# Kernel optimization log

Measured on AMD Instinct MI355X. Metric: run time of the kernel, lower is better.

## Reference

```python
import jax, jax.numpy as jnp
import numpy as np

# Config (matches AttentionConfig)
B, T, D = 2, 2048, 2048
H, KV, HD = 32, 8, 64          # n_heads, n_kv_heads, head_dim = d_model // n_heads
GROUPS = H // KV               # 4 query heads share each KV head
THETA = 10000.0
SCALE = 1.0 / np.sqrt(HD)
EPS = 1e-6


def setup_inputs() -> dict:
    key = jax.random.key(0)
    ks = jax.random.split(key, 6)
    def xavier(k, fan_in, fan_out):
        limit = np.sqrt(6.0 / (fan_in + fan_out))
        return jax.random.uniform(k, (fan_in, fan_out), jnp.float32, -limit, limit)
    return {
        "x": jax.random.normal(ks[0], (B, T, D), jnp.float32),
        "Wq": xavier(ks[1], D, H * HD),
        "Wk": xavier(ks[2], D, KV * HD),
        "Wv": xavier(ks[3], D, KV * HD),
        "Wo": xavier(ks[4], H * HD, D),
        "q_scale": jnp.ones((HD,), jnp.float32),
        "k_scale": jnp.ones((HD,), jnp.float32),
    }


def _rmsnorm(x, scale):
    # per-head RMSNorm over last dim (head_dim)
    rms = jnp.sqrt(jnp.mean(jnp.square(x), axis=-1, keepdims=True) + EPS)
    return (x / rms) * scale


def _rope(x):
    # x: (B, T, h, HD); rotate-half RoPE, offset=0
    pos = jnp.arange(x.shape[1], dtype=jnp.float32)
    inv_freq = 1.0 / (THETA ** (jnp.arange(0, HD, 2, dtype=jnp.float32) / HD))
    ang = pos[:, None] * inv_freq[None, :]          # (T, HD/2)
    cos = jnp.cos(ang)[None, :, None, :]
    sin = jnp.sin(ang)[None, :, None, :]
    x1, x2 = x[..., : HD // 2], x[..., HD // 2 :]
    return jnp.concatenate([x1 * cos - x2 * sin, x2 * cos + x1 * sin], axis=-1)


def reference(x, Wq, Wk, Wv, Wo, q_scale, k_scale):
    # projections -> (B, T, heads, HD)
    q = (x @ Wq).reshape(B, T, H, HD)
    k = (x @ Wk).reshape(B, T, KV, HD)
    v = (x @ Wv).reshape(B, T, KV, HD)
    # per-head QK RMSNorm (applied before RoPE, as in the module)
    q = _rmsnorm(q, q_scale)
    k = _rmsnorm(k, k_scale)
    # RoPE on q and k
    q = _rope(q)
    k = _rope(k)
    # repeat KV heads: head index = kv_head * GROUPS + g (matches _repeat_kv)
    k = jnp.repeat(k, GROUPS, axis=2)   # (B, T, H, HD)
    v = jnp.repeat(v, GROUPS, axis=2)
    # attention scores (B, H, T, T)
    logits = jnp.einsum("bqhd,bkhd->bhqk", q, k) * SCALE
    causal = jnp.triu(jnp.ones((T, T), bool), k=1)  # True = masked
    logits = jnp.where(causal[None, None], -jnp.inf, logits)
    w = jax.nn.softmax(logits, axis=-1)
    w = jnp.nan_to_num(w)
    out = jnp.einsum("bhqk,bkhd->bqhd", w, v).reshape(B, T, H * HD)
    return out @ Wo
```

## Files before the change

### kernel.cpp

```cpp
#include <hip/hip_runtime.h>
#include <hip/hip_bf16.h>

typedef __attribute__((ext_vector_type(4))) float f32x4;
typedef __attribute__((ext_vector_type(8))) short bf16x8;
typedef __attribute__((ext_vector_type(4))) short short4v;

#define DEVI __device__ __forceinline__

constexpr int Bc = 2, Tc = 2048, Dc = 2048, Hc = 32, KVc = 8, HDc = 64;
constexpr int GRP = Hc / KVc;
constexpr float EPSc = 1e-6f;
constexpr float QMULT = 0.125f * 1.4426950408889634f;
constexpr float INV2PI = 0.15915494309189535f;
constexpr float ROPE_C = 0.41524101186092029f;

DEVI short f2b(float f) {
    __hip_bfloat16 h = __float2bfloat16(f);
    short s;
    __builtin_memcpy(&s, &h, sizeof(short));
    return s;
}
DEVI float b2f(short s) {
    unsigned int u = ((unsigned int)(unsigned short)s) << 16;
    float f;
    __builtin_memcpy(&f, &u, sizeof(float));
    return f;
}

#define GLOAD16(g, l)                                                        \
    __builtin_amdgcn_global_load_lds(                                        \
        (const __attribute__((address_space(1))) void*)(g),                  \
        (__attribute__((address_space(3))) void*)(l), 16, 0, 0)

__global__ __launch_bounds__(256) void prep_all(const float* __restrict__ x,
                                                const float* __restrict__ Wq,
                                                const float* __restrict__ Wk,
                                                const float* __restrict__ Wv,
                                                const float* __restrict__ Wo,
                                                short* __restrict__ xb,
                                                short* __restrict__ WqkvT,
                                                short* __restrict__ WoT) {
    const int z = blockIdx.z;
    if (z == 4) {
        size_t base = ((size_t)(blockIdx.y * 32 + blockIdx.x) * 256 + threadIdx.x) * 8;
#pragma unroll
        for (int p = 0; p < 4; ++p) {
            size_t i = base + (size_t)p * 2097152;
            float4 a = *reinterpret_cast<const float4*>(x + i);
            float4 b = *reinterpret_cast<const float4*>(x + i + 4);
            bf16x8 o = {f2b(a.x), f2b(a.y), f2b(a.z), f2b(a.w),
                        f2b(b.x), f2b(b.y), f2b(b.z), f2b(b.w)};
            *reinterpret_cast<bf16x8*>(xb + i) = o;
        }
        return;
    }
    const float* src;
    short* dst;
    int C;
    if (z == 0)      { src = Wq; dst = WqkvT;                          C = 2048; }
    else if (z == 1) { src = Wk; dst = WqkvT + (size_t)2048 * 2048;    C = 512; }
    else if (z == 2) { src = Wv; dst = WqkvT + (size_t)2560 * 2048;    C = 512; }
    else             { src = Wo; dst = WoT;                            C = 2048; }
    const int n0 = blockIdx.x * 64, k0 = blockIdx.y * 64;
    if (n0 >= C) return;

    __shared__ __align__(16) short t[64][72];
    const int rl = threadIdx.x >> 2, q = threadIdx.x & 3;
#pragma unroll
    for (int jj = 0; jj < 4; ++jj) {
        float4 v = *reinterpret_cast<const float4*>(src + (size_t)(k0 + rl) * C + n0 + q * 16 + jj * 4);
        short4v s = {f2b(v.x), f2b(v.y), f2b(v.z), f2b(v.w)};
        *reinterpret_cast<short4v*>(&t[rl][q * 16 + jj * 4]) = s;
    }
    __syncthreads();
    alignas(16) short buf[16];
#pragma unroll
    for (int e = 0; e < 16; ++e) buf[e] = t[q * 16 + e][rl];
    short* d = dst + (size_t)(n0 + rl) * 2048 + k0 + q * 16;
    *reinterpret_cast<int4*>(d) = reinterpret_cast<int4*>(buf)[0];
    *reinterpret_cast<int4*>(d + 8) = reinterpret_cast<int4*>(buf)[1];
}

DEVI void xcd_swizzle(int nx, int& bx, int& by) {
    int nwg = nx * gridDim.y;
    int fb = by * nx + bx;
    int cpx = nwg >> 3;
    int swz = (fb & 7) * cpx + (fb >> 3);
    by = swz / nx;
    bx = swz - by * nx;
}

__global__ __launch_bounds__(256) void gemm_proj(const short* __restrict__ A,
                                                 const short* __restrict__ Bt,
                                                 const float* __restrict__ qs,
                                                 const float* __restrict__ ks,
                                                 short* __restrict__ qb,
                                                 short* __restrict__ kb,
                                                 short* __restrict__ vt) {
    constexpr int K = 2048;
    __shared__ __align__(16) short sA[2][128 * 64];
    __shared__ __align__(16) short sB[2][128 * 64];

    const int tid = threadIdx.x;
    const int wave = tid >> 6, lane = tid & 63;
    const int lhi = lane >> 4, llo = lane & 15;
    int bx = blockIdx.x, by = blockIdx.y;
    xcd_swizzle(24, bx, by);
    const int bm = by * 128, bn = bx * 128;
    const int wm = (wave >> 1) * 64, wn = (wave & 1) * 64;

    const short* apt[4];
    const short* bpt[4];
#pragma unroll
    for (int l = 0; l < 4; ++l) {
        int c = l * 256 + tid;
        int r = c >> 3, ck = (c & 7) ^ (r & 7);
        apt[l] = A + (size_t)(bm + r) * K + ck * 8;
        bpt[l] = Bt + (size_t)(bn + r) * K + ck * 8;
    }

    f32x4 acc[4][4] = {};

#pragma unroll
    for (int l = 0; l < 4; ++l) {
        GLOAD16(apt[l], &sA[0][(l * 256 + tid) * 8]);
        GLOAD16(bpt[l], &sB[0][(l * 256 + tid) * 8]);
    }
    int c = 0;
    const int co0 = ((lhi ^ (llo & 7)) << 3);
    const int co1 = (((4 + lhi) ^ (llo & 7)) << 3);

#pragma unroll 1
    for (int k0 = 0; k0 < K; k0 += 64) {
        if (k0 + 64 < K) {
            const int kn = k0 + 64;
#pragma unroll
            for (int l = 0; l < 4; ++l) {
                GLOAD16(apt[l] + kn, &sA[c ^ 1][(l * 256 + tid) * 8]);
                GLOAD16(bpt[l] + kn, &sB[c ^ 1][(l * 256 + tid) * 8]);
            }
            asm volatile("s_waitcnt vmcnt(8)" ::: "memory");
        } else {
            asm volatile("s_waitcnt vmcnt(0)" ::: "memory");
        }
        __builtin_amdgcn_s_barrier();
        asm volatile("" ::: "memory");

#pragma unroll
        for (int kk = 0; kk < 2; ++kk) {
            const int co = kk ? co1 : co0;
            bf16x8 af[4], bf[4];
#pragma unroll
            for (int i = 0; i < 4; ++i)
                af[i] = *reinterpret_cast<const bf16x8*>(&sA[c][(wm + i * 16 + llo) * 64 + co]);
#pragma unroll
            for (int j = 0; j < 4; ++j)
                bf[j] = *reinterpret_cast<const bf16x8*>(&sB[c][(wn + j * 16 + llo) * 64 + co]);
#pragma unroll
            for (int i = 0; i < 4; ++i)
#pragma unroll
                for (int j = 0; j < 4; ++j)
                    acc[i][j] = __builtin_amdgcn_mfma_f32_16x16x32_bf16(af[i], bf[j], acc[i][j], 0, 0, 0);
        }

        asm volatile("" ::: "memory");
        __builtin_amdgcn_s_barrier();
        c ^= 1;
    }

    const int rm = bm + wm;
    const int b = rm >> 11;
    const int tb = rm & 2047;
    const int col0 = bn + wn;

    if (col0 < 2560) {
        const bool isq = col0 < 2048;
        const float* scale = isq ? qs : ks;
        const float mult = isq ? QMULT : 1.0f;
        float scl[4];
#pragma unroll
        for (int j = 0; j < 4; ++j) scl[j] = scale[j * 16 + llo];
        short* outp;
        if (isq)
            outp = qb + (size_t)(b * Hc + (col0 >> 6)) * 2048 * 64;
        else
            outp = kb + (size_t)(b * KVc + ((col0 - 2048) >> 6)) * 2048 * 64;
        const float ir0 = INV2PI * exp2f(-ROPE_C * (float)llo);
        const float ir1 = INV2PI * exp2f(-ROPE_C * (float)(16 + llo));
#pragma unroll
        for (int i = 0; i < 4; ++i)
#pragma unroll
            for (int r = 0; r < 4; ++r) {
                float ss = 0.f;
#pragma unroll
                for (int j = 0; j < 4; ++j) ss += acc[i][j][r] * acc[i][j][r];
                ss += __shfl_xor(ss, 1);
                ss += __shfl_xor(ss, 2);
                ss += __shfl_xor(ss, 4);
                ss += __shfl_xor(ss, 8);
                float rinv = 1.0f / sqrtf(ss * (1.0f / 64.0f) + EPSc);
                float vn[4];
#pragma unroll
                for (int j = 0; j < 4; ++j) vn[j] = acc[i][j][r] * rinv * scl[j];
                const int t = tb + i * 16 + lhi * 4 + r;
                float f0 = (float)t * ir0;
                f0 -= floorf(f0);
                float f1 = (float)t * ir1;
                f1 -= floorf(f1);
                float sn0 = __builtin_amdgcn_sinf(f0), cs0 = __builtin_amdgcn_cosf(f0);
                float sn1 = __builtin_amdgcn_sinf(f1), cs1 = __builtin_amdgcn_cosf(f1);
                size_t base = (size_t)t * 64 + llo;
                outp[base]      = f2b((vn[0] * cs0 - vn[2] * sn0) * mult);
                outp[base + 16] = f2b((vn[1] * cs1 - vn[3] * sn1) * mult);
                outp[base + 32] = f2b((vn[2] * cs0 + vn[0] * sn0) * mult);
                outp[base + 48] = f2b((vn[3] * cs1 + vn[1] * sn1) * mult);
            }
    } else {
        const int kv = (col0 - 2560) >> 6;
        const int tile = tb >> 6;
        short* dst = vt + ((size_t)(b * 8 + kv) * 32 + tile) * 4096;
#pragma unroll
        for (int i = 0; i < 4; ++i)
#pragma unroll
            for (int j = 0; j < 4; ++j) {
                short4v p4 = {f2b(acc[i][j][0]), f2b(acc[i][j][1]),
                              f2b(acc[i][j][2]), f2b(acc[i][j][3])};
                *reinterpret_cast<short4v*>(
                    &dst[(j * 16 + llo) * 64 + i * 16 + lhi * 4]) = p4;
            }
    }
}

template <typename CT>
__global__ __launch_bounds__(256) void gemm_bt(const short* __restrict__ A,
                                               const short* __restrict__ Bt,
                                               CT* __restrict__ C, int M, int N, int K) {
    __shared__ __align__(16) short sA[2][128 * 64];
    __shared__ __align__(16) short sB[2][128 * 64];

    const int tid = threadIdx.x;
    const int wave = tid >> 6, lane = tid & 63;
    const int lhi = lane >> 4, llo = lane & 15;
    int bx = blockIdx.x, by = blockIdx.y;
    xcd_swizzle(gridDim.x, bx, by);
    const int bm = by * 128, bn = bx * 128;
    const int wm = (wave >> 1) * 64, wn = (wave & 1) * 64;

    const short* apt[4];
    const short* bpt[4];
#pragma unroll
    for (int l = 0; l < 4; ++l) {
        int c = l * 256 + tid;
        int r = c >> 3, ck = (c & 7) ^ (r & 7);
        apt[l] = A + (size_t)(bm + r) * K + ck * 8;
        bpt[l] = Bt + (size_t)(bn + r) * K + ck * 8;
    }

    f32x4 acc[4][4] = {};

#pragma unroll
    for (int l = 0; l < 4; ++l) {
        GLOAD16(apt[l], &sA[0][(l * 256 + tid) * 8]);
        GLOAD16(bpt[l], &sB[0][(l * 256 + tid) * 8]);
    }
    int c = 0;
    const int co0 = ((lhi ^ (llo & 7)) << 3);
    const int co1 = (((4 + lhi) ^ (llo & 7)) << 3);

#pragma unroll 1
    for (int k0 = 0; k0 < K; k0 += 64) {
        if (k0 + 64 < K) {
            const int kn = k0 + 64;
#pragma unroll
            for (int l = 0; l < 4; ++l) {
                GLOAD16(apt[l] + kn, &sA[c ^ 1][(l * 256 + tid) * 8]);
                GLOAD16(bpt[l] + kn, &sB[c ^ 1][(l * 256 + tid) * 8]);
            }
            asm volatile("s_waitcnt vmcnt(8)" ::: "memory");
        } else {
            asm volatile("s_waitcnt vmcnt(0)" ::: "memory");
        }
        __builtin_amdgcn_s_barrier();
        asm volatile("" ::: "memory");

#pragma unroll
        for (int kk = 0; kk < 2; ++kk) {
            const int co = kk ? co1 : co0;
            bf16x8 af[4], bf[4];
#pragma unroll
            for (int i = 0; i < 4; ++i)
                af[i] = *reinterpret_cast<const bf16x8*>(&sA[c][(wm + i * 16 + llo) * 64 + co]);
#pragma unroll
            for (int j = 0; j < 4; ++j)
                bf[j] = *reinterpret_cast<const bf16x8*>(&sB[c][(wn + j * 16 + llo) * 64 + co]);
#pragma unroll
            for (int i = 0; i < 4; ++i)
#pragma unroll
                for (int j = 0; j < 4; ++j)
                    acc[i][j] = __builtin_amdgcn_mfma_f32_16x16x32_bf16(af[i], bf[j], acc[i][j], 0, 0, 0);
        }

        asm volatile("" ::: "memory");
        __builtin_amdgcn_s_barrier();
        c ^= 1;
    }

#pragma unroll
    for (int i = 0; i < 4; ++i)
#pragma unroll
        for (int j = 0; j < 4; ++j)
#pragma unroll
            for (int r = 0; r < 4; ++r) {
                size_t idx = (size_t)(bm + wm + i * 16 + lhi * 4 + r) * N + bn + wn + j * 16 + llo;
                if constexpr (sizeof(CT) == 2)
                    C[idx] = f2b(acc[i][j][r]);
                else
                    C[idx] = acc[i][j][r];
            }
}

__global__ __launch_bounds__(256) void attn_fwd(const short* __restrict__ Qb,
                                                const short* __restrict__ Kb,
                                                const short* __restrict__ Vt,
                                                short* __restrict__ Ob) {
    __shared__ __align__(16) short sK[2][64 * 64];
    __shared__ __align__(16) short sV[2][64 * 64];
    __shared__ __align__(16) short sP[4][32 * 72];

    const int hb = blockIdx.x;
    const int qt = 15 - (int)blockIdx.y;
    const int h = hb & 31, b = hb >> 5;
    const int kvh = h >> 2;
    const int tid = threadIdx.x, wave = tid >> 6, lane = tid & 63;
    const int lhi = lane >> 4, llo = lane & 15;

    const short* Qp = Qb + (size_t)(b * Hc + h) * Tc * 64;
    const short* Kp = Kb + (size_t)(b * KVc + kvh) * Tc * 64;
    const short* Vp = Vt + (size_t)(b * KVc + kvh) * 32 * 4096;

    const int srow0 = tid >> 3, sslot0 = tid & 7;
    const int srow1 = (256 + tid) >> 3, sslot1 = tid & 7;
    const int soff0 = (sslot0 ^ (srow0 & 7)) * 8;
    const int soff1 = (sslot1 ^ (srow1 & 7)) * 8;

    const int Q0 = qt * 128 + wave * 32;
    const int ktmax_w = (Q0 + 31) >> 6;
    const int nkt = 2 * qt + 2;

    bf16x8 qf[2][2];
#pragma unroll
    for (int q16 = 0; q16 < 2; ++q16)
#pragma unroll
        for (int kk = 0; kk < 2; ++kk)
            qf[q16][kk] = *reinterpret_cast<const bf16x8*>(
                Qp + (size_t)(Q0 + q16 * 16 + llo) * 64 + kk * 32 + lhi * 8);

    f32x4 o[2][4] = {};
    float mreg[2] = {-1e30f, -1e30f};
    float lreg[2] = {0.f, 0.f};

    {
        GLOAD16(Kp + (size_t)srow0 * 64 + soff0, &sK[0][tid * 8]);
        GLOAD16(Vp + (size_t)srow0 * 64 + soff0, &sV[0][tid * 8]);
        GLOAD16(Kp + (size_t)srow1 * 64 + soff1, &sK[0][(256 + tid) * 8]);
        GLOAD16(Vp + (size_t)srow1 * 64 + soff1, &sV[0][(256 + tid) * 8]);
    }
    int c = 0;

#pragma unroll 1
    for (int kt = 0; kt < nkt; ++kt) {
        const bool has_next = (kt + 1) < nkt;
        if (has_next) {
            const size_t kbase = (size_t)(kt + 1) * 4096;
            GLOAD16(Kp + kbase + srow0 * 64 + soff0, &sK[c ^ 1][tid * 8]);
            GLOAD16(Vp + kbase + srow0 * 64 + soff0, &sV[c ^ 1][tid * 8]);
            GLOAD16(Kp + kbase + srow1 * 64 + soff1, &sK[c ^ 1][(256 + tid) * 8]);
            GLOAD16(Vp + kbase + srow1 * 64 + soff1, &sV[c ^ 1][(256 + tid) * 8]);
            asm volatile("s_waitcnt vmcnt(4)" ::: "memory");
        } else {
            asm volatile("s_waitcnt vmcnt(0)" ::: "memory");
        }
        __builtin_amdgcn_s_barrier();
        asm volatile("" ::: "memory");

        if (kt <= ktmax_w) {
            const short* sKc = sK[c];
            const short* sVc = sV[c];
            f32x4 st[2][4];
            __builtin_amdgcn_s_setprio(1);
#pragma unroll
            for (int n = 0; n < 4; ++n) {
                int krow = n * 16 + llo;
                bf16x8 ka0 = *reinterpret_cast<const bf16x8*>(
                    &sKc[krow * 64 + ((lhi ^ (krow & 7)) << 3)]);
                bf16x8 ka1 = *reinterpret_cast<const bf16x8*>(
                    &sKc[krow * 64 + (((4 + lhi) ^ (krow & 7)) << 3)]);
                f32x4 z = {0.f, 0.f, 0.f, 0.f};
                st[0][n] = __builtin_amdgcn_mfma_f32_16x16x32_bf16(ka0, qf[0][0], z, 0, 0, 0);
                st[0][n] = __builtin_amdgcn_mfma_f32_16x16x32_bf16(ka1, qf[0][1], st[0][n], 0, 0, 0);
                st[1][n] = __builtin_amdgcn_mfma_f32_16x16x32_bf16(ka0, qf[1][0], z, 0, 0, 0);
                st[1][n] = __builtin_amdgcn_mfma_f32_16x16x32_bf16(ka1, qf[1][1], st[1][n], 0, 0, 0);
            }
            __builtin_amdgcn_s_setprio(0);
            if (kt == ktmax_w) {
#pragma unroll
                for (int q16 = 0; q16 < 2; ++q16) {
                    int qg = Q0 + q16 * 16 + llo;
#pragma unroll
                    for (int n = 0; n < 4; ++n)
#pragma unroll
                        for (int r = 0; r < 4; ++r) {
                            int kvg = kt * 64 + n * 16 + lhi * 4 + r;
                            if (kvg > qg) st[q16][n][r] = -1e30f;
                        }
                }
            }
            float pm[2];
#pragma unroll
            for (int q16 = 0; q16 < 2; ++q16) {
                float r0 = fmaxf(fmaxf(st[q16][0][0], st[q16][0][1]),
                                 fmaxf(st[q16][0][2], st[q16][0][3]));
                float r1 = fmaxf(fmaxf(st[q16][1][0], st[q16][1][1]),
                                 fmaxf(st[q16][1][2], st[q16][1][3]));
                float r2 = fmaxf(fmaxf(st[q16][2][0], st[q16][2][1]),
                                 fmaxf(st[q16][2][2], st[q16][2][3]));
                float r3 = fmaxf(fmaxf(st[q16][3][0], st[q16][3][1]),
                                 fmaxf(st[q16][3][2], st[q16][3][3]));
                float p = fmaxf(fmaxf(r0, r1), fmaxf(r2, r3));
                p = fmaxf(p, __shfl_xor(p, 16));
                p = fmaxf(p, __shfl_xor(p, 32));
                pm[q16] = p;
            }
            bool defer = __all((pm[0] - mreg[0] <= 8.f) && (pm[1] - mreg[1] <= 8.f));
            if (!defer) {
                float alpha[2];
#pragma unroll
                for (int q16 = 0; q16 < 2; ++q16) {
                    float mn = fmaxf(mreg[q16], pm[q16]);
                    alpha[q16] = __builtin_amdgcn_exp2f(mreg[q16] - mn);
                    mreg[q16] = mn;
                    lreg[q16] *= alpha[q16];
                }
#pragma unroll
                for (int q16 = 0; q16 < 2; ++q16)
#pragma unroll
                    for (int r = 0; r < 4; ++r) {
                        float ar = __shfl(alpha[q16], lhi * 4 + r);
#pragma unroll
                        for (int j = 0; j < 4; ++j) o[q16][j][r] *= ar;
                    }
            }
#pragma unroll
            for (int q16 = 0; q16 < 2; ++q16) {
                float ps = 0.f;
#pragma unroll
                for (int n = 0; n < 4; ++n)
#pragma unroll
                    for (int r = 0; r < 4; ++r) {
                        float p = __builtin_amdgcn_exp2f(st[q16][n][r] - mreg[q16]);
                        st[q16][n][r] = p;
                        ps += p;
                    }
                ps += __shfl_xor(ps, 16);
                ps += __shfl_xor(ps, 32);
                lreg[q16] += ps;
            }
#pragma unroll
            for (int q16 = 0; q16 < 2; ++q16)
#pragma unroll
                for (int n = 0; n < 4; ++n) {
                    short4v p4 = {f2b(st[q16][n][0]), f2b(st[q16][n][1]),
                                  f2b(st[q16][n][2]), f2b(st[q16][n][3])};
                    *reinterpret_cast<short4v*>(
                        &sP[wave][(q16 * 16 + llo) * 72 + n * 16 + lhi * 4]) = p4;
                }
            __builtin_amdgcn_s_setprio(1);
#pragma unroll
            for (int kk = 0; kk < 2; ++kk) {
                bf16x8 pa0 = *reinterpret_cast<const bf16x8*>(
                    &sP[wave][(0 * 16 + llo) * 72 + kk * 32 + lhi * 8]);
                bf16x8 pa1 = *reinterpret_cast<const bf16x8*>(
                    &sP[wave][(1 * 16 + llo) * 72 + kk * 32 + lhi * 8]);
#pragma unroll
                for (int j = 0; j < 4; ++j) {
                    int vrow = j * 16 + llo;
                    bf16x8 vf = *reinterpret_cast<const bf16x8*>(
                        &sVc[vrow * 64 + ((((kk * 4) + lhi) ^ (vrow & 7)) << 3)]);
                    o[0][j] = __builtin_amdgcn_mfma_f32_16x16x32_bf16(pa0, vf, o[0][j], 0, 0, 0);
                    o[1][j] = __builtin_amdgcn_mfma_f32_16x16x32_bf16(pa1, vf, o[1][j], 0, 0, 0);
                }
            }
            __builtin_amdgcn_s_setprio(0);
        }
        asm volatile("" ::: "memory");
        __builtin_amdgcn_s_barrier();
        c ^= 1;
    }

#pragma unroll
    for (int q16 = 0; q16 < 2; ++q16) {
        float inv = 1.0f / lreg[q16];
#pragma unroll
        for (int r = 0; r < 4; ++r) {
            float ivr = __shfl(inv, lhi * 4 + r);
            int qrow = Q0 + q16 * 16 + lhi * 4 + r;
#pragma unroll
            for (int j = 0; j < 4; ++j)
                Ob[((size_t)(b * Tc + qrow)) * 2048 + h * 64 + j * 16 + llo] =
                    f2b(o[q16][j][r] * ivr);
        }
    }
}

extern "C" void kernel_launch(void* const* d_in, const int* in_sizes, int n_in,
                              void* d_out, int out_size, void* d_ws, size_t ws_size,
                              hipStream_t stream) {
    const float* x  = (const float*)d_in[0];
    const float* Wq = (const float*)d_in[1];
    const float* Wk = (const float*)d_in[2];
    const float* Wv = (const float*)d_in[3];
    const float* Wo = (const float*)d_in[4];
    const float* qs = (const float*)d_in[5];
    const float* ks = (const float*)d_in[6];
    float* out = (float*)d_out;

    char* w = (char*)d_ws;
    short* xb    = (short*)(w);
    short* WqkvT = (short*)(w + 16777216);
    short* WoT   = (short*)(w + 29360128);
    short* vt    = (short*)(w + 37748736);
    short* qb    = (short*)(w + 62914560);
    short* kb    = (short*)(w + 79691776);
    short* ob    = xb;

    dim3 blk(256);
    prep_all<<<dim3(32, 32, 5), blk, 0, stream>>>(x, Wq, Wk, Wv, Wo, xb, WqkvT, WoT);
    gemm_proj<<<dim3(24, 32), blk, 0, stream>>>(xb, WqkvT, qs, ks, qb, kb, vt);
    attn_fwd<<<dim3(64, 16), blk, 0, stream>>>(qb, kb, vt, ob);
    gemm_bt<float><<<dim3(16, 32), blk, 0, stream>>>(ob, WoT, out, 4096, 2048, 2048);
}
```

Measured before the change: 218.5 us.

## Transpose attention probabilities via cross-lane shuffles instead of LDS staging

Replaces the per-wave shared-memory round trip for the softmax probability tile (write as C layout, read back as A-operand layout) with in-register bf16 packing and __shfl-based lane permutation. It also drops the sP LDS buffer and adds a min-blocks-per-CU hint of 4 to launch bounds. The aim is to cut LDS traffic and the store-load latency on the inner loop and free LDS for occupancy. The cost is more shuffle instructions (each a ds_bpermute) plus selects, and possible register pressure from the occupancy hint.

```diff
diff --git a/kernel.cpp b/kernel.cpp
--- a/kernel.cpp
+++ b/kernel.cpp
@@ -319,13 +319,12 @@
             }
 }
 
-__global__ __launch_bounds__(256) void attn_fwd(const short* __restrict__ Qb,
-                                                const short* __restrict__ Kb,
-                                                const short* __restrict__ Vt,
-                                                short* __restrict__ Ob) {
+__global__ __launch_bounds__(256, 4) void attn_fwd(const short* __restrict__ Qb,
+                                                   const short* __restrict__ Kb,
+                                                   const short* __restrict__ Vt,
+                                                   short* __restrict__ Ob) {
     __shared__ __align__(16) short sK[2][64 * 64];
     __shared__ __align__(16) short sV[2][64 * 64];
-    __shared__ __align__(16) short sP[4][32 * 72];
 
     const int hb = blockIdx.x;
     const int qt = 15 - (int)blockIdx.y;
@@ -346,6 +345,10 @@
     const int Q0 = qt * 128 + wave * 32;
     const int ktmax_w = (Q0 + 31) >> 6;
     const int nkt = 2 * qt + 2;
+
+    const int src0 = llo + ((lhi & 1) << 5);
+    const int src1 = src0 + 16;
+    const bool nsel = (lhi & 2) != 0;
 
     bf16x8 qf[2][2];
 #pragma unroll
@@ -465,22 +468,34 @@
                 ps += __shfl_xor(ps, 32);
                 lreg[q16] += ps;
             }
-#pragma unroll
-            for (int q16 = 0; q16 < 2; ++q16)
-#pragma unroll
-                for (int n = 0; n < 4; ++n) {
-                    short4v p4 = {f2b(st[q16][n][0]), f2b(st[q16][n][1]),
-                                  f2b(st[q16][n][2]), f2b(st[q16][n][3])};
-                    *reinterpret_cast<short4v*>(
-                        &sP[wave][(q16 * 16 + llo) * 72 + n * 16 + lhi * 4]) = p4;
-                }
+            unsigned w0[2][4], w1[2][4];
+#pragma unroll
+            for (int q16 = 0; q16 < 2; ++q16) {
+                unsigned pk[4][2];
+#pragma unroll
+                for (int n = 0; n < 4; ++n)
+#pragma unroll
+                    for (int p = 0; p < 2; ++p)
+                        pk[n][p] = (unsigned)(unsigned short)f2b(st[q16][n][2 * p]) |
+                                   ((unsigned)(unsigned short)f2b(st[q16][n][2 * p + 1]) << 16);
+#pragma unroll
+                for (int kk = 0; kk < 2; ++kk)
+#pragma unroll
+                    for (int e2 = 0; e2 < 4; ++e2) {
+                        int src = (e2 < 2) ? src0 : src1;
+                        unsigned lo = __shfl((int)pk[2 * kk + 0][e2 & 1], src);
+                        unsigned hi = __shfl((int)pk[2 * kk + 1][e2 & 1], src);
+                        unsigned v = nsel ? hi : lo;
+                        if (q16 == 0) w0[kk][e2] = v;
+                        else          w1[kk][e2] = v;
+                    }
+            }
             __builtin_amdgcn_s_setprio(1);
 #pragma unroll
             for (int kk = 0; kk < 2; ++kk) {
-                bf16x8 pa0 = *reinterpret_cast<const bf16x8*>(
-                    &sP[wave][(0 * 16 + llo) * 72 + kk * 32 + lhi * 8]);
-                bf16x8 pa1 = *reinterpret_cast<const bf16x8*>(
-                    &sP[wave][(1 * 16 + llo) * 72 + kk * 32 + lhi * 8]);
+                bf16x8 pa0, pa1;
+                __builtin_memcpy(&pa0, w0[kk], 16);
+                __builtin_memcpy(&pa1, w1[kk], 16);
 #pragma unroll
                 for (int j = 0; j < 4; ++j) {
                     int vrow = j * 16 + llo;
```

After: 246.5 us. +12.8%, slower.

## Split attention work across eight waves of sixteen query rows each

Applied to the files above, without the earlier changes.

The attention kernel moves from 256 threads with 4 waves, each handling 32 query rows, to 512 threads with 8 waves, each handling 16 rows. Each thread now issues one K and one V tile load per stage, and the per-wave softmax state and accumulators shrink. The goal is more wave-level parallelism and lower register pressure for better latency hiding. In exchange, each wave reads the K/V fragments from LDS for only 16 rows instead of 32, which raises LDS traffic per unit of MFMA work, and blocks become larger.

```diff
diff --git a/kernel.cpp b/kernel.cpp
--- a/kernel.cpp
+++ b/kernel.cpp
@@ -319,13 +319,13 @@
             }
 }
 
-__global__ __launch_bounds__(256) void attn_fwd(const short* __restrict__ Qb,
+__global__ __launch_bounds__(512) void attn_fwd(const short* __restrict__ Qb,
                                                 const short* __restrict__ Kb,
                                                 const short* __restrict__ Vt,
                                                 short* __restrict__ Ob) {
     __shared__ __align__(16) short sK[2][64 * 64];
     __shared__ __align__(16) short sV[2][64 * 64];
-    __shared__ __align__(16) short sP[4][32 * 72];
+    __shared__ __align__(16) short sP[8][16 * 72];
 
     const int hb = blockIdx.x;
     const int qt = 15 - (int)blockIdx.y;
@@ -338,32 +338,26 @@
     const short* Kp = Kb + (size_t)(b * KVc + kvh) * Tc * 64;
     const short* Vp = Vt + (size_t)(b * KVc + kvh) * 32 * 4096;
 
-    const int srow0 = tid >> 3, sslot0 = tid & 7;
-    const int srow1 = (256 + tid) >> 3, sslot1 = tid & 7;
-    const int soff0 = (sslot0 ^ (srow0 & 7)) * 8;
-    const int soff1 = (sslot1 ^ (srow1 & 7)) * 8;
-
-    const int Q0 = qt * 128 + wave * 32;
-    const int ktmax_w = (Q0 + 31) >> 6;
+    const int srow = tid >> 3, sslot = tid & 7;
+    const int soff = (sslot ^ (srow & 7)) * 8;
+
+    const int Q0 = qt * 128 + wave * 16;
+    const int ktmax_w = (Q0 + 15) >> 6;
     const int nkt = 2 * qt + 2;
 
-    bf16x8 qf[2][2];
-#pragma unroll
-    for (int q16 = 0; q16 < 2; ++q16)
-#pragma unroll
-        for (int kk = 0; kk < 2; ++kk)
-            qf[q16][kk] = *reinterpret_cast<const bf16x8*>(
-                Qp + (size_t)(Q0 + q16 * 16 + llo) * 64 + kk * 32 + lhi * 8);
-
-    f32x4 o[2][4] = {};
-    float mreg[2] = {-1e30f, -1e30f};
-    float lreg[2] = {0.f, 0.f};
+    bf16x8 qf[2];
+#pragma unroll
+    for (int kk = 0; kk < 2; ++kk)
+        qf[kk] = *reinterpret_cast<const bf16x8*>(
+            Qp + (size_t)(Q0 + llo) * 64 + kk * 32 + lhi * 8);
+
+    f32x4 o[4] = {};
+    float mreg = -1e30f;
+    float lreg = 0.f;
 
     {
-        GLOAD16(Kp + (size_t)srow0 * 64 + soff0, &sK[0][tid * 8]);
-        GLOAD16(Vp + (size_t)srow0 * 64 + soff0, &sV[0][tid * 8]);
-        GLOAD16(Kp + (size_t)srow1 * 64 + soff1, &sK[0][(256 + tid) * 8]);
-        GLOAD16(Vp + (size_t)srow1 * 64 + soff1, &sV[0][(256 + tid) * 8]);
+        GLOAD16(Kp + (size_t)srow * 64 + soff, &sK[0][tid * 8]);
+        GLOAD16(Vp + (size_t)srow * 64 + soff, &sV[0][tid * 8]);
     }
     int c = 0;
 
@@ -372,11 +366,9 @@
         const bool has_next = (kt + 1) < nkt;
         if (has_next) {
             const size_t kbase = (size_t)(kt + 1) * 4096;
-            GLOAD16(Kp + kbase + srow0 * 64 + soff0, &sK[c ^ 1][tid * 8]);
-            GLOAD16(Vp + kbase + srow0 * 64 + soff0, &sV[c ^ 1][tid * 8]);
-            GLOAD16(Kp + kbase + srow1 * 64 + soff1, &sK[c ^ 1][(256 + tid) * 8]);
-            GLOAD16(Vp + kbase + srow1 * 64 + soff1, &sV[c ^ 1][(256 + tid) * 8]);
-            asm volatile("s_waitcnt vmcnt(4)" ::: "memory");
+            GLOAD16(Kp + kbase + srow * 64 + soff, &sK[c ^ 1][tid * 8]);
+            GLOAD16(Vp + kbase + srow * 64 + soff, &sV[c ^ 1][tid * 8]);
+            asm volatile("s_waitcnt vmcnt(2)" ::: "memory");
         } else {
             asm volatile("s_waitcnt vmcnt(0)" ::: "memory");
         }
@@ -386,7 +378,7 @@
         if (kt <= ktmax_w) {
             const short* sKc = sK[c];
             const short* sVc = sV[c];
-            f32x4 st[2][4];
+            f32x4 st[4];
             __builtin_amdgcn_s_setprio(1);
 #pragma unroll
             for (int n = 0; n < 4; ++n) {
@@ -396,98 +388,68 @@
                 bf16x8 ka1 = *reinterpret_cast<const bf16x8*>(
                     &sKc[krow * 64 + (((4 + lhi) ^ (krow & 7)) << 3)]);
                 f32x4 z = {0.f, 0.f, 0.f, 0.f};
-                st[0][n] = __builtin_amdgcn_mfma_f32_16x16x32_bf16(ka0, qf[0][0], z, 0, 0, 0);
-                st[0][n] = __builtin_amdgcn_mfma_f32_16x16x32_bf16(ka1, qf[0][1], st[0][n], 0, 0, 0);
-                st[1][n] = __builtin_amdgcn_mfma_f32_16x16x32_bf16(ka0, qf[1][0], z, 0, 0, 0);
-                st[1][n] = __builtin_amdgcn_mfma_f32_16x16x32_bf16(ka1, qf[1][1], st[1][n], 0, 0, 0);
+                st[n] = __builtin_amdgcn_mfma_f32_16x16x32_bf16(ka0, qf[0], z, 0, 0, 0);
+                st[n] = __builtin_amdgcn_mfma_f32_16x16x32_bf16(ka1, qf[1], st[n], 0, 0, 0);
             }
             __builtin_amdgcn_s_setprio(0);
             if (kt == ktmax_w) {
-#pragma unroll
-                for (int q16 = 0; q16 < 2; ++q16) {
-                    int qg = Q0 + q16 * 16 + llo;
-#pragma unroll
-                    for (int n = 0; n < 4; ++n)
-#pragma unroll
-                        for (int r = 0; r < 4; ++r) {
-                            int kvg = kt * 64 + n * 16 + lhi * 4 + r;
-                            if (kvg > qg) st[q16][n][r] = -1e30f;
-                        }
+                int qg = Q0 + llo;
+#pragma unroll
+                for (int n = 0; n < 4; ++n)
+#pragma unroll
+                    for (int r = 0; r < 4; ++r) {
+                        int kvg = kt * 64 + n * 16 + lhi * 4 + r;
+                        if (kvg > qg) st[n][r] = -1e30f;
+                    }
+            }
+            float r0 = fmaxf(fmaxf(st[0][0], st[0][1]), fmaxf(st[0][2], st[0][3]));
+            float r1 = fmaxf(fmaxf(st[1][0], st[1][1]), fmaxf(st[1][2], st[1][3]));
+            float r2 = fmaxf(fmaxf(st[2][0], st[2][1]), fmaxf(st[2][2], st[2][3]));
+            float r3 = fmaxf(fmaxf(st[3][0], st[3][1]), fmaxf(st[3][2], st[3][3]));
+            float pm = fmaxf(fmaxf(r0, r1), fmaxf(r2, r3));
+            pm = fmaxf(pm, __shfl_xor(pm, 16));
+            pm = fmaxf(pm, __shfl_xor(pm, 32));
+            bool defer = __all(pm - mreg <= 8.f);
+            if (!defer) {
+                float mn = fmaxf(mreg, pm);
+                float alpha = __builtin_amdgcn_exp2f(mreg - mn);
+                mreg = mn;
+                lreg *= alpha;
+#pragma unroll
+                for (int r = 0; r < 4; ++r) {
+                    float ar = __shfl(alpha, lhi * 4 + r);
+#pragma unroll
+                    for (int j = 0; j < 4; ++j) o[j][r] *= ar;
                 }
             }
-            float pm[2];
-#pragma unroll
-            for (int q16 = 0; q16 < 2; ++q16) {
-                float r0 = fmaxf(fmaxf(st[q16][0][0], st[q16][0][1]),
-                                 fmaxf(st[q16][0][2], st[q16][0][3]));
-                float r1 = fmaxf(fmaxf(st[q16][1][0], st[q16][1][1]),
-                                 fmaxf(st[q16][1][2], st[q16][1][3]));
-                float r2 = fmaxf(fmaxf(st[q16][2][0], st[q16][2][1]),
-                                 fmaxf(st[q16][2][2], st[q16][2][3]));
-                float r3 = fmaxf(fmaxf(st[q16][3][0], st[q16][3][1]),
-                                 fmaxf(st[q16][3][2], st[q16][3][3]));
-                float p = fmaxf(fmaxf(r0, r1), fmaxf(r2, r3));
-                p = fmaxf(p, __shfl_xor(p, 16));
-                p = fmaxf(p, __shfl_xor(p, 32));
-                pm[q16] = p;
-            }
-            bool defer = __all((pm[0] - mreg[0] <= 8.f) && (pm[1] - mreg[1] <= 8.f));
-            if (!defer) {
-                float alpha[2];
-#pragma unroll
-                for (int q16 = 0; q16 < 2; ++q16) {
-                    float mn = fmaxf(mreg[q16], pm[q16]);
-                    alpha[q16] = __builtin_amdgcn_exp2f(mreg[q16] - mn);
-                    mreg[q16] = mn;
-                    lreg[q16] *= alpha[q16];
+            float ps = 0.f;
+#pragma unroll
+            for (int n = 0; n < 4; ++n)
+#pragma unroll
+                for (int r = 0; r < 4; ++r) {
+                    float p = __builtin_amdgcn_exp2f(st[n][r] - mreg);
+                    st[n][r] = p;
+                    ps += p;
                 }
-#pragma unroll
-                for (int q16 = 0; q16 < 2; ++q16)
-#pragma unroll
-                    for (int r = 0; r < 4; ++r) {
-                        float ar = __shfl(alpha[q16], lhi * 4 + r);
-#pragma unroll
-                        for (int j = 0; j < 4; ++j) o[q16][j][r] *= ar;
-                    }
-            }
-#pragma unroll
-            for (int q16 = 0; q16 < 2; ++q16) {
-                float ps = 0.f;
-#pragma unroll
-                for (int n = 0; n < 4; ++n)
-#pragma unroll
-                    for (int r = 0; r < 4; ++r) {
-                        float p = __builtin_amdgcn_exp2f(st[q16][n][r] - mreg[q16]);
-                        st[q16][n][r] = p;
-                        ps += p;
-                    }
-                ps += __shfl_xor(ps, 16);
-                ps += __shfl_xor(ps, 32);
-                lreg[q16] += ps;
-            }
-#pragma unroll
-            for (int q16 = 0; q16 < 2; ++q16)
-#pragma unroll
-                for (int n = 0; n < 4; ++n) {
-                    short4v p4 = {f2b(st[q16][n][0]), f2b(st[q16][n][1]),
-                                  f2b(st[q16][n][2]), f2b(st[q16][n][3])};
-                    *reinterpret_cast<short4v*>(
-                        &sP[wave][(q16 * 16 + llo) * 72 + n * 16 + lhi * 4]) = p4;
-                }
+            ps += __shfl_xor(ps, 16);
+            ps += __shfl_xor(ps, 32);
+            lreg += ps;
+#pragma unroll
+            for (int n = 0; n < 4; ++n) {
+                short4v p4 = {f2b(st[n][0]), f2b(st[n][1]), f2b(st[n][2]), f2b(st[n][3])};
+                *reinterpret_cast<short4v*>(&sP[wave][llo * 72 + n * 16 + lhi * 4]) = p4;
+            }
             __builtin_amdgcn_s_setprio(1);
 #pragma unroll
             for (int kk = 0; kk < 2; ++kk) {
-                bf16x8 pa0 = *reinterpret_cast<const bf16x8*>(
-                    &sP[wave][(0 * 16 + llo) * 72 + kk * 32 + lhi * 8]);
-                bf16x8 pa1 = *reinterpret_cast<const bf16x8*>(
-                    &sP[wave][(1 * 16 + llo) * 72 + kk * 32 + lhi * 8]);
+                bf16x8 pa = *reinterpret_cast<const bf16x8*>(
+                    &sP[wave][llo * 72 + kk * 32 + lhi * 8]);
 #pragma unroll
                 for (int j = 0; j < 4; ++j) {
                     int vrow = j * 16 + llo;
                     bf16x8 vf = *reinterpret_cast<const bf16x8*>(
                         &sVc[vrow * 64 + ((((kk * 4) + lhi) ^ (vrow & 7)) << 3)]);
-                    o[0][j] = __builtin_amdgcn_mfma_f32_16x16x32_bf16(pa0, vf, o[0][j], 0, 0, 0);
-                    o[1][j] = __builtin_amdgcn_mfma_f32_16x16x32_bf16(pa1, vf, o[1][j], 0, 0, 0);
+                    o[j] = __builtin_amdgcn_mfma_f32_16x16x32_bf16(pa, vf, o[j], 0, 0, 0);
                 }
             }
             __builtin_amdgcn_s_setprio(0);
@@ -497,17 +459,16 @@
         c ^= 1;
     }
 
-#pragma unroll
-    for (int q16 = 0; q16 < 2; ++q16) {
-        float inv = 1.0f / lreg[q16];
+    {
+        float inv = 1.0f / lreg;
 #pragma unroll
         for (int r = 0; r < 4; ++r) {
             float ivr = __shfl(inv, lhi * 4 + r);
-            int qrow = Q0 + q16 * 16 + lhi * 4 + r;
+            int qrow = Q0 + lhi * 4 + r;
 #pragma unroll
             for (int j = 0; j < 4; ++j)
                 Ob[((size_t)(b * Tc + qrow)) * 2048 + h * 64 + j * 16 + llo] =
-                    f2b(o[q16][j][r] * ivr);
+                    f2b(o[j][r] * ivr);
         }
     }
 }
@@ -536,6 +497,6 @@
     dim3 blk(256);
     prep_all<<<dim3(32, 32, 5), blk, 0, stream>>>(x, Wq, Wk, Wv, Wo, xb, WqkvT, WoT);
     gemm_proj<<<dim3(24, 32), blk, 0, stream>>>(xb, WqkvT, qs, ks, qb, kb, vt);
-    attn_fwd<<<dim3(64, 16), blk, 0, stream>>>(qb, kb, vt, ob);
+    attn_fwd<<<dim3(64, 16), dim3(512), 0, stream>>>(qb, kb, vt, ob);
     gemm_bt<float><<<dim3(16, 32), blk, 0, stream>>>(ob, WoT, out, 4096, 2048, 2048);
 }
```

After: 203.7 us. 6.8% less time.
